# Kernel optimization log

Measured on AMD Instinct MI355X. Metric: run time of the kernel, lower is better.

## Reference

```python
import jax, jax.numpy as jnp
import numpy as np

DELTA_HEADING = 15.0
DELTA_BEARING = 15.0
N_HEADING = int(360 // 15)  # 24
N_BEARING = int(360 // 15)  # 24
MASK_FILL = 1e24


def setup_inputs() -> dict:
    key = jax.random.key(0)
    k1, k2, k3, k4, k5, k6 = jax.random.split(key, 6)
    N, B, H = 128, 256, 128
    hidden_state = jax.random.normal(k1, (N, B, H), dtype=jnp.float32)
    # distances in a realistic positive range
    distance_matrix = jax.random.uniform(k2, (B, N, N), dtype=jnp.float32, minval=0.0, maxval=10.0)
    bearing_matrix = jax.random.uniform(k3, (B, N, N), dtype=jnp.float32, minval=0.0, maxval=360.0)
    heading_matrix = jax.random.uniform(k4, (B, N, N), dtype=jnp.float32, minval=0.0, maxval=360.0)
    # mostly-valid sequence mask (bool, per batch x vessel)
    sequence_mask = jax.random.uniform(k5, (B, N)) > 0.1
    domain = jax.random.normal(k6, (N_HEADING, N_BEARING), dtype=jnp.float32)
    return {
        "hidden_state": hidden_state,
        "distance_matrix": distance_matrix,
        "bearing_matrix": bearing_matrix,
        "heading_matrix": heading_matrix,
        "sequence_mask": sequence_mask,
        "domain": domain,
    }


def reference(hidden_state, distance_matrix, bearing_matrix, heading_matrix, sequence_mask, domain):
    # indices into learned domain table
    idx1 = jnp.clip(jnp.floor(heading_matrix / DELTA_HEADING), 0, N_HEADING - 1).astype(jnp.int32)
    idx2 = jnp.clip(jnp.floor(bearing_matrix / DELTA_BEARING), 0, N_BEARING - 1).astype(jnp.int32)
    # pairwise validity mask: (B,N,1) & (B,1,N)
    wmask = sequence_mask[:, :, None] & sequence_mask[:, None, :]
    dist = jnp.where(wmask, distance_matrix, MASK_FILL)
    weights = jax.nn.softplus(domain[idx1, idx2] - dist)  # (B,N,N)
    # hidden_state: (N,B,H) -> (B,N,H); weighted sum over neighbors j
    h = jnp.swapaxes(hidden_state, 0, 1)
    weighted_hidden = jnp.tanh(jnp.einsum('bij,bjh->bih', weights, h))
    weighted_hidden = jnp.where(sequence_mask[:, :, None], weighted_hidden, 0.0)
    return weighted_hidden
```

## Files before the change

### kernel.cpp

```cpp
#include <hip/hip_runtime.h>

#define NV 128
#define NB 256
#define NH 128
#define KC 32
#define HSTR 40

typedef __attribute__((ext_vector_type(8))) unsigned short ushort8;
typedef __attribute__((ext_vector_type(4))) float f32x4;
typedef __attribute__((ext_vector_type(8))) __bf16 bf16x8;

__device__ __forceinline__ unsigned short f2bf(float x) {
  unsigned u = __builtin_bit_cast(unsigned, x);
  return (unsigned short)((u + 0x7fffu + ((u >> 16) & 1u)) >> 16);
}
__device__ __forceinline__ float bf2f(unsigned short h) {
  return __builtin_bit_cast(float, (unsigned)h << 16);
}

__launch_bounds__(256, 2)
__global__ void spatial_attn_mfma(const float* __restrict__ hidden,
                                  const float* __restrict__ dist,
                                  const float* __restrict__ brg,
                                  const float* __restrict__ hdg,
                                  const unsigned char* __restrict__ maskraw,
                                  const float* __restrict__ domain,
                                  float* __restrict__ out) {
  __shared__ unsigned short thi[2][NH * HSTR];
  __shared__ unsigned short tlo[2][NH * HSTR];
  __shared__ float dom[24 * 24];
  __shared__ float maskf[NV];
  __shared__ int kindsh;

  const int tid = threadIdx.x;
  const int lane = tid & 63;
  const int wv = tid >> 6;
  const int b = blockIdx.x >> 1;
  const int ih = (blockIdx.x & 1) * 64;

  for (int k = tid; k < 576; k += 256) dom[k] = domain[k];
  if (tid == 0) kindsh = 1;
  const unsigned char s1 = maskraw[(size_t)(b & 63) * 512 + 4 * (tid & 127) + 1];
  __syncthreads();
  if (s1 != 0) kindsh = 0;
  __syncthreads();
  if (tid < NV) {
    const int m = kindsh ? ((const int*)maskraw)[b * NV + tid]
                         : (int)maskraw[b * NV + tid];
    maskf[tid] = (m != 0) ? 1.0f : 0.0f;
  }
  __syncthreads();

  const int fm = lane & 15;
  const int j0 = (lane >> 4) * 8;
  const int arow = ih + 16 * wv + fm;

  f32x4 acc[8];
#pragma unroll
  for (int t = 0; t < 8; ++t) acc[t] = (f32x4)0.0f;

  const float* dR = dist + ((size_t)b * NV + arow) * NV;
  const float* bR = brg + ((size_t)b * NV + arow) * NV;
  const float* gR = hdg + ((size_t)b * NV + arow) * NV;

  const int shh = tid & 127;
  const int sjh = (tid >> 7) * 16;

#define STAGE_H(cc, bb)                                                       \
  {                                                                           \
    const int jb = (cc) * KC + sjh;                                           \
    float v[16];                                                              \
    _Pragma("unroll") for (int k = 0; k < 16; ++k)                            \
        v[k] = hidden[((size_t)(jb + k) * NB + b) * NH + shh];                \
    ushort8 ph0, ph1, pl0, pl1;                                               \
    _Pragma("unroll") for (int k = 0; k < 8; ++k) {                           \
      const unsigned short h = f2bf(v[k]);                                    \
      ph0[k] = h;                                                             \
      pl0[k] = f2bf(v[k] - bf2f(h));                                          \
    }                                                                         \
    _Pragma("unroll") for (int k = 0; k < 8; ++k) {                           \
      const unsigned short h = f2bf(v[8 + k]);                                \
      ph1[k] = h;                                                             \
      pl1[k] = f2bf(v[8 + k] - bf2f(h));                                      \
    }                                                                         \
    *(ushort8*)&thi[bb][shh * HSTR + sjh] = ph0;                              \
    *(ushort8*)&thi[bb][shh * HSTR + sjh + 8] = ph1;                          \
    *(ushort8*)&tlo[bb][shh * HSTR + sjh] = pl0;                              \
    *(ushort8*)&tlo[bb][shh * HSTR + sjh + 8] = pl1;                          \
  }

  STAGE_H(0, 0);

  float4 pd0 = *(const float4*)&dR[j0];
  float4 pd1 = *(const float4*)&dR[j0 + 4];
  float4 pb0 = *(const float4*)&bR[j0];
  float4 pb1 = *(const float4*)&bR[j0 + 4];
  float4 pg0 = *(const float4*)&gR[j0];
  float4 pg1 = *(const float4*)&gR[j0 + 4];

  for (int cs = 0; cs < 4; ++cs) {
    const int jc = cs * KC;
    const int cb = cs & 1;

    const float dv[8] = {pd0.x, pd0.y, pd0.z, pd0.w, pd1.x, pd1.y, pd1.z, pd1.w};
    const float bv[8] = {pb0.x, pb0.y, pb0.z, pb0.w, pb1.x, pb1.y, pb1.z, pb1.w};
    const float gv[8] = {pg0.x, pg0.y, pg0.z, pg0.w, pg1.x, pg1.y, pg1.z, pg1.w};

    if (cs < 3) {
      const int jn = (cs + 1) * KC + j0;
      pd0 = *(const float4*)&dR[jn];
      pd1 = *(const float4*)&dR[jn + 4];
      pb0 = *(const float4*)&bR[jn];
      pb1 = *(const float4*)&bR[jn + 4];
      pg0 = *(const float4*)&gR[jn];
      pg1 = *(const float4*)&gR[jn + 4];
      STAGE_LOAD_NEXT:;
    }

    ushort8 ahi_u, alo_u;
#pragma unroll
    for (int e = 0; e < 8; ++e) {
      const int i1 = min(23, max(0, (int)floorf(gv[e] * (1.0f / 15.0f))));
      const int i2 = min(23, max(0, (int)floorf(bv[e] * (1.0f / 15.0f))));
      const float t = dom[i1 * 24 + i2] - dv[e];
      const float sp = fmaxf(t, 0.0f) + __logf(1.0f + __expf(-fabsf(t)));
      const float w = sp * maskf[jc + j0 + e];
      const unsigned short h = f2bf(w);
      ahi_u[e] = h;
      alo_u[e] = f2bf(w - bf2f(h));
    }
    const bf16x8 ahi = __builtin_bit_cast(bf16x8, ahi_u);
    const bf16x8 alo = __builtin_bit_cast(bf16x8, alo_u);

    float hv[16];
    if (cs < 3) {
      const int jb = (cs + 1) * KC + sjh;
#pragma unroll
      for (int k = 0; k < 16; ++k)
        hv[k] = hidden[((size_t)(jb + k) * NB + b) * NH + shh];
    }

    __syncthreads();
    if (cs < 3) {
      ushort8 ph0, ph1, pl0, pl1;
#pragma unroll
      for (int k = 0; k < 8; ++k) {
        const unsigned short h = f2bf(hv[k]);
        ph0[k] = h;
        pl0[k] = f2bf(hv[k] - bf2f(h));
      }
#pragma unroll
      for (int k = 0; k < 8; ++k) {
        const unsigned short h = f2bf(hv[8 + k]);
        ph1[k] = h;
        pl1[k] = f2bf(hv[8 + k] - bf2f(h));
      }
      const int bb = cb ^ 1;
      *(ushort8*)&thi[bb][shh * HSTR + sjh] = ph0;
      *(ushort8*)&thi[bb][shh * HSTR + sjh + 8] = ph1;
      *(ushort8*)&tlo[bb][shh * HSTR + sjh] = pl0;
      *(ushort8*)&tlo[bb][shh * HSTR + sjh + 8] = pl1;
    }

#pragma unroll
    for (int t = 0; t < 8; ++t) {
      const int boff = (16 * t + fm) * HSTR + j0;
      const bf16x8 bhi = __builtin_bit_cast(bf16x8, *(const ushort8*)&thi[cb][boff]);
      const bf16x8 blo = __builtin_bit_cast(bf16x8, *(const ushort8*)&tlo[cb][boff]);
      acc[t] = __builtin_amdgcn_mfma_f32_16x16x32_bf16(ahi, bhi, acc[t], 0, 0, 0);
      acc[t] = __builtin_amdgcn_mfma_f32_16x16x32_bf16(ahi, blo, acc[t], 0, 0, 0);
      acc[t] = __builtin_amdgcn_mfma_f32_16x16x32_bf16(alo, bhi, acc[t], 0, 0, 0);
    }
  }

  float* oB = out + (size_t)b * NV * NH;
  const int rbase = ih + 16 * wv + 4 * (lane >> 4);
#pragma unroll
  for (int t = 0; t < 8; ++t) {
    const int hh = 16 * t + fm;
#pragma unroll
    for (int r = 0; r < 4; ++r) {
      const int i = rbase + r;
      const float x = acc[t][r];
      const float ex = __expf(2.0f * x);
      const float th = 1.0f - __fdividef(2.0f, ex + 1.0f);
      oB[i * NH + hh] = th * maskf[i];
    }
  }
}

extern "C" void kernel_launch(void* const* d_in, const int* in_sizes, int n_in,
                              void* d_out, int out_size, void* d_ws, size_t ws_size,
                              hipStream_t stream) {
  const float* hidden = (const float*)d_in[0];
  const float* dist = (const float*)d_in[1];
  const float* brg = (const float*)d_in[2];
  const float* hdg = (const float*)d_in[3];
  const unsigned char* mask = (const unsigned char*)d_in[4];
  const float* domain = (const float*)d_in[5];
  float* out = (float*)d_out;

  spatial_attn_mfma<<<NB * 2, 256, 0, stream>>>(hidden, dist, brg, hdg, mask,
                                                domain, out);
}
```

Baseline: 25.02 us.

## Process one batch per 512-thread block, staging full hidden tile in LDS once

The launch changes from two 256-thread blocks per batch to one 512-thread block per batch, with 8 waves covering all 128 output rows. The whole hidden slice for the batch is converted to split bf16 hi/lo and staged into LDS once, replacing the double-buffered per-chunk staging and its per-iteration barriers. Each batch's hidden data is now read from global memory once instead of twice, and three of the four chunk barriers go away. In exchange, the up-front staging no longer overlaps with MFMA work, LDS use per block grows, and occupancy drops to one large block per CU.

```diff
diff --git a/kernel.cpp b/kernel.cpp
--- a/kernel.cpp
+++ b/kernel.cpp
@@ -4,7 +4,7 @@
 #define NB 256
 #define NH 128
 #define KC 32
-#define HSTR 40
+#define HSTR 136
 
 typedef __attribute__((ext_vector_type(8))) unsigned short ushort8;
 typedef __attribute__((ext_vector_type(4))) float f32x4;
@@ -18,7 +18,7 @@
   return __builtin_bit_cast(float, (unsigned)h << 16);
 }
 
-__launch_bounds__(256, 2)
+__launch_bounds__(512, 1)
 __global__ void spatial_attn_mfma(const float* __restrict__ hidden,
                                   const float* __restrict__ dist,
                                   const float* __restrict__ brg,
@@ -26,8 +26,8 @@
                                   const unsigned char* __restrict__ maskraw,
                                   const float* __restrict__ domain,
                                   float* __restrict__ out) {
-  __shared__ unsigned short thi[2][NH * HSTR];
-  __shared__ unsigned short tlo[2][NH * HSTR];
+  __shared__ unsigned short thi[NH * HSTR];
+  __shared__ unsigned short tlo[NH * HSTR];
   __shared__ float dom[24 * 24];
   __shared__ float maskf[NV];
   __shared__ int kindsh;
@@ -35,10 +35,9 @@
   const int tid = threadIdx.x;
   const int lane = tid & 63;
   const int wv = tid >> 6;
-  const int b = blockIdx.x >> 1;
-  const int ih = (blockIdx.x & 1) * 64;
+  const int b = blockIdx.x;
 
-  for (int k = tid; k < 576; k += 256) dom[k] = domain[k];
+  for (int k = tid; k < 576; k += 512) dom[k] = domain[k];
   if (tid == 0) kindsh = 1;
   const unsigned char s1 = maskraw[(size_t)(b & 63) * 512 + 4 * (tid & 127) + 1];
   __syncthreads();
@@ -49,47 +48,44 @@
                          : (int)maskraw[b * NV + tid];
     maskf[tid] = (m != 0) ? 1.0f : 0.0f;
   }
-  __syncthreads();
+
+  {
+    const int shh = tid & 127;
+    const int sj = (tid >> 7) * 32;
+#pragma unroll
+    for (int g = 0; g < 2; ++g) {
+      const int jb = sj + g * 16;
+      float v[16];
+#pragma unroll
+      for (int k = 0; k < 16; ++k)
+        v[k] = hidden[((size_t)(jb + k) * NB + b) * NH + shh];
+      ushort8 ph0, ph1, pl0, pl1;
+#pragma unroll
+      for (int k = 0; k < 8; ++k) {
+        const unsigned short h = f2bf(v[k]);
+        ph0[k] = h;
+        pl0[k] = f2bf(v[k] - bf2f(h));
+      }
+#pragma unroll
+      for (int k = 0; k < 8; ++k) {
+        const unsigned short h = f2bf(v[8 + k]);
+        ph1[k] = h;
+        pl1[k] = f2bf(v[8 + k] - bf2f(h));
+      }
+      *(ushort8*)&thi[shh * HSTR + jb] = ph0;
+      *(ushort8*)&thi[shh * HSTR + jb + 8] = ph1;
+      *(ushort8*)&tlo[shh * HSTR + jb] = pl0;
+      *(ushort8*)&tlo[shh * HSTR + jb + 8] = pl1;
+    }
+  }
 
   const int fm = lane & 15;
   const int j0 = (lane >> 4) * 8;
-  const int arow = ih + 16 * wv + fm;
-
-  f32x4 acc[8];
-#pragma unroll
-  for (int t = 0; t < 8; ++t) acc[t] = (f32x4)0.0f;
+  const int arow = 16 * wv + fm;
 
   const float* dR = dist + ((size_t)b * NV + arow) * NV;
   const float* bR = brg + ((size_t)b * NV + arow) * NV;
   const float* gR = hdg + ((size_t)b * NV + arow) * NV;
-
-  const int shh = tid & 127;
-  const int sjh = (tid >> 7) * 16;
-
-#define STAGE_H(cc, bb)                                                       \
-  {                                                                           \
-    const int jb = (cc) * KC + sjh;                                           \
-    float v[16];                                                              \
-    _Pragma("unroll") for (int k = 0; k < 16; ++k)                            \
-        v[k] = hidden[((size_t)(jb + k) * NB + b) * NH + shh];                \
-    ushort8 ph0, ph1, pl0, pl1;                                               \
-    _Pragma("unroll") for (int k = 0; k < 8; ++k) {                           \
-      const unsigned short h = f2bf(v[k]);                                    \
-      ph0[k] = h;                                                             \
-      pl0[k] = f2bf(v[k] - bf2f(h));                                          \
-    }                                                                         \
-    _Pragma("unroll") for (int k = 0; k < 8; ++k) {                           \
-      const unsigned short h = f2bf(v[8 + k]);                                \
-      ph1[k] = h;                                                             \
-      pl1[k] = f2bf(v[8 + k] - bf2f(h));                                      \
-    }                                                                         \
-    *(ushort8*)&thi[bb][shh * HSTR + sjh] = ph0;                              \
-    *(ushort8*)&thi[bb][shh * HSTR + sjh + 8] = ph1;                          \
-    *(ushort8*)&tlo[bb][shh * HSTR + sjh] = pl0;                              \
-    *(ushort8*)&tlo[bb][shh * HSTR + sjh + 8] = pl1;                          \
-  }
-
-  STAGE_H(0, 0);
 
   float4 pd0 = *(const float4*)&dR[j0];
   float4 pd1 = *(const float4*)&dR[j0 + 4];
@@ -98,9 +94,15 @@
   float4 pg0 = *(const float4*)&gR[j0];
   float4 pg1 = *(const float4*)&gR[j0 + 4];
 
+  f32x4 acc[8];
+#pragma unroll
+  for (int t = 0; t < 8; ++t) acc[t] = (f32x4)0.0f;
+
+  __syncthreads();
+
+#pragma unroll
   for (int cs = 0; cs < 4; ++cs) {
     const int jc = cs * KC;
-    const int cb = cs & 1;
 
     const float dv[8] = {pd0.x, pd0.y, pd0.z, pd0.w, pd1.x, pd1.y, pd1.z, pd1.w};
     const float bv[8] = {pb0.x, pb0.y, pb0.z, pb0.w, pb1.x, pb1.y, pb1.z, pb1.w};
@@ -114,7 +116,6 @@
       pb1 = *(const float4*)&bR[jn + 4];
       pg0 = *(const float4*)&gR[jn];
       pg1 = *(const float4*)&gR[jn + 4];
-      STAGE_LOAD_NEXT:;
     }
 
     ushort8 ahi_u, alo_u;
@@ -132,41 +133,11 @@
     const bf16x8 ahi = __builtin_bit_cast(bf16x8, ahi_u);
     const bf16x8 alo = __builtin_bit_cast(bf16x8, alo_u);
 
-    float hv[16];
-    if (cs < 3) {
-      const int jb = (cs + 1) * KC + sjh;
-#pragma unroll
-      for (int k = 0; k < 16; ++k)
-        hv[k] = hidden[((size_t)(jb + k) * NB + b) * NH + shh];
-    }
-
-    __syncthreads();
-    if (cs < 3) {
-      ushort8 ph0, ph1, pl0, pl1;
-#pragma unroll
-      for (int k = 0; k < 8; ++k) {
-        const unsigned short h = f2bf(hv[k]);
-        ph0[k] = h;
-        pl0[k] = f2bf(hv[k] - bf2f(h));
-      }
-#pragma unroll
-      for (int k = 0; k < 8; ++k) {
-        const unsigned short h = f2bf(hv[8 + k]);
-        ph1[k] = h;
-        pl1[k] = f2bf(hv[8 + k] - bf2f(h));
-      }
-      const int bb = cb ^ 1;
-      *(ushort8*)&thi[bb][shh * HSTR + sjh] = ph0;
-      *(ushort8*)&thi[bb][shh * HSTR + sjh + 8] = ph1;
-      *(ushort8*)&tlo[bb][shh * HSTR + sjh] = pl0;
-      *(ushort8*)&tlo[bb][shh * HSTR + sjh + 8] = pl1;
-    }
-
 #pragma unroll
     for (int t = 0; t < 8; ++t) {
-      const int boff = (16 * t + fm) * HSTR + j0;
-      const bf16x8 bhi = __builtin_bit_cast(bf16x8, *(const ushort8*)&thi[cb][boff]);
-      const bf16x8 blo = __builtin_bit_cast(bf16x8, *(const ushort8*)&tlo[cb][boff]);
+      const int boff = (16 * t + fm) * HSTR + jc + j0;
+      const bf16x8 bhi = __builtin_bit_cast(bf16x8, *(const ushort8*)&thi[boff]);
+      const bf16x8 blo = __builtin_bit_cast(bf16x8, *(const ushort8*)&tlo[boff]);
       acc[t] = __builtin_amdgcn_mfma_f32_16x16x32_bf16(ahi, bhi, acc[t], 0, 0, 0);
       acc[t] = __builtin_amdgcn_mfma_f32_16x16x32_bf16(ahi, blo, acc[t], 0, 0, 0);
       acc[t] = __builtin_amdgcn_mfma_f32_16x16x32_bf16(alo, bhi, acc[t], 0, 0, 0);
@@ -174,7 +145,7 @@
   }
 
   float* oB = out + (size_t)b * NV * NH;
-  const int rbase = ih + 16 * wv + 4 * (lane >> 4);
+  const int rbase = 16 * wv + 4 * (lane >> 4);
 #pragma unroll
   for (int t = 0; t < 8; ++t) {
     const int hh = 16 * t + fm;
@@ -200,6 +171,6 @@
   const float* domain = (const float*)d_in[5];
   float* out = (float*)d_out;
 
-  spatial_attn_mfma<<<NB * 2, 256, 0, stream>>>(hidden, dist, brg, hdg, mask,
-                                                domain, out);
+  spatial_attn_mfma<<<NB, 512, 0, stream>>>(hidden, dist, brg, hdg, mask,
+                                            domain, out);
 }
```

New measurement: 24.47 us. 1.02x faster.
